# Kernel optimization log

Hardware: AMD Instinct MI355X
Metric: run time of the kernel (lower is better)

The kernel has to match this reference:

```python
import jax, jax.numpy as jnp
import numpy as np

B, D, H = 131072, 8, 128  # batch, input_size (condition dims), hidden_size
DROPOUT_PROB = 0.1
NAN_FRAC = 0.15


def setup_inputs() -> dict:
    key = jax.random.key(0)
    k1, k2, k3, k4, k5, k6 = jax.random.split(key, 6)
    labels = jax.random.normal(k1, (B, D), dtype=jnp.float32)
    # NaN marks 'missing condition' -> falls back to embedding table row
    nan_mask = jax.random.uniform(k2, (B, D)) < NAN_FRAC
    labels = jnp.where(nan_mask, jnp.nan, labels)
    emb_w = jax.random.normal(k3, (D, H), dtype=jnp.float32) * 0.02  # embedding_drop.weight
    w1 = jax.random.normal(k4, (D, H), dtype=jnp.float32)           # Linear(1,H).weight per dim
    b1 = jax.random.normal(k5, (D, H), dtype=jnp.float32) * 0.02    # Linear(1,H).bias per dim
    w2 = jax.random.normal(k6, (D, H, H), dtype=jnp.float32) * 0.08 # Linear(H,H,bias=False).weight [out,in]
    return {"labels": labels, "emb_w": emb_w, "w1": w1, "b1": b1, "w2": w2,
            "train": 0, "unconditioned": 0}


def reference(labels, emb_w, w1, b1, w2, train, unconditioned):
    # drop mask per (sample, dim): NaN labels, optional random dropout, or everything
    if unconditioned:
        drop = jnp.ones(labels.shape, dtype=bool)
    else:
        drop = jnp.isnan(labels)
        if train:
            rkey = jax.random.fold_in(jax.random.key(0), 1)
            drop = drop | (jax.random.uniform(rkey, labels.shape) < DROPOUT_PROB)
    safe = jnp.where(drop, 0.0, labels)                      # [B,D] NaN-free
    # per-dim MLP, vectorized over dims: Linear(1,H) -> softmax(H) -> Linear(H,H)
    h1 = safe[:, :, None] * w1[None, :, :] + b1[None, :, :]  # [B,D,H]
    s = jax.nn.softmax(h1, axis=-1)                          # softmax over hidden (dim=1 of [N,H])
    mlp = jnp.einsum('bdh,dkh->bdk', s, w2)                  # [B,D,H]
    emb = jnp.where(drop[:, :, None], emb_w[None, :, :], mlp)
    if train:
        nkey = jax.random.fold_in(jax.random.key(0), 2)
        emb = emb + jax.random.normal(nkey, emb.shape, dtype=emb.dtype)
    return emb.sum(axis=1)                                   # [B,H]
```

## Files before the change

### kernel.cpp

```cpp
#include <hip/hip_runtime.h>
#include <hip/hip_bf16.h>

typedef __attribute__((ext_vector_type(4))) float f32x4;
typedef __attribute__((ext_vector_type(4))) int   i32x4;
typedef __attribute__((ext_vector_type(8))) short s16x8;

#define NB 131072
#define ND 8
#define NH 128
#define BROWS 128

#if __has_builtin(__builtin_amdgcn_exp2f)
#define EXP2F(x) __builtin_amdgcn_exp2f(x)
#define PRESCALE 1.4426950408889634f
#else
#define EXP2F(x) __expf(x)
#define PRESCALE 1.0f
#endif

#if __has_builtin(__builtin_amdgcn_rcpf)
#define RCPF(x) __builtin_amdgcn_rcpf(x)
#else
#define RCPF(x) (1.0f / (x))
#endif

__device__ __forceinline__ unsigned short f2bf(float f){
  unsigned u = __float_as_uint(f);
  u += 0x7fffu + ((u >> 16) & 1u);
  return (unsigned short)(u >> 16);
}

__device__ __forceinline__ unsigned pk2(float lo, float hi){
  return __builtin_amdgcn_perm(__float_as_uint(hi), __float_as_uint(lo), 0x07060302u);
}

__global__ __launch_bounds__(256) void cvt_w2_kernel(const float* __restrict__ src,
                                                     uint4* __restrict__ dst){
  int i = blockIdx.x * 256 + threadIdx.x;
  int d = i >> 11, kb = (i >> 7) & 15, n = i & 127;
  const float* s = src + ((d * 128 + n) * 128 + kb * 8);
  float4 v0 = ((const float4*)s)[0];
  float4 v1 = ((const float4*)s)[1];
  uint4 o;
  o.x = (unsigned)f2bf(v0.x) | ((unsigned)f2bf(v0.y) << 16);
  o.y = (unsigned)f2bf(v0.z) | ((unsigned)f2bf(v0.w) << 16);
  o.z = (unsigned)f2bf(v1.x) | ((unsigned)f2bf(v1.y) << 16);
  o.w = (unsigned)f2bf(v1.z) | ((unsigned)f2bf(v1.w) << 16);
  dst[i] = o;
}

__global__ __launch_bounds__(256, 3) void cond_embed_kernel(
    const float* __restrict__ labels,
    const float* __restrict__ emb_w,
    const float* __restrict__ w1,
    const float* __restrict__ b1,
    const unsigned short* __restrict__ w2b,
    const int* __restrict__ uncond_p,
    float* __restrict__ out)
{
  __shared__ __align__(16) unsigned short lds_w2[NH * NH];
  __shared__ __align__(16) float lds_lab[ND * BROWS];
  __shared__ __align__(16) float lds_w1[ND * NH];
  __shared__ __align__(16) float lds_b1[ND * NH];
  __shared__ __align__(16) unsigned short lds_embT[NH * 8];

  const int tid  = threadIdx.x;
  const int wave = tid >> 6;
  const int lane = tid & 63;
  const int quad = lane >> 4;
  const int l16  = lane & 15;
  const int uncond = uncond_p[0];
  const int blockbase = blockIdx.x * BROWS;

  {
    float4 v = ((const float4*)(labels + blockbase * ND))[tid];
    int row = tid >> 1, dbase = (tid & 1) * 4;
    lds_lab[(dbase + 0) * BROWS + row] = v.x;
    lds_lab[(dbase + 1) * BROWS + row] = v.y;
    lds_lab[(dbase + 2) * BROWS + row] = v.z;
    lds_lab[(dbase + 3) * BROWS + row] = v.w;
  }
  {
    float4 a = ((const float4*)w1)[tid];
    float4 b = ((const float4*)b1)[tid];
    ((float4*)lds_w1)[tid] = (float4){a.x * PRESCALE, a.y * PRESCALE, a.z * PRESCALE, a.w * PRESCALE};
    ((float4*)lds_b1)[tid] = (float4){b.x * PRESCALE, b.y * PRESCALE, b.z * PRESCALE, b.w * PRESCALE};
  }
  if (tid < NH){
    unsigned e0 = f2bf(emb_w[0*NH + tid]), e1 = f2bf(emb_w[1*NH + tid]);
    unsigned e2 = f2bf(emb_w[2*NH + tid]), e3 = f2bf(emb_w[3*NH + tid]);
    unsigned e4 = f2bf(emb_w[4*NH + tid]), e5 = f2bf(emb_w[5*NH + tid]);
    unsigned e6 = f2bf(emb_w[6*NH + tid]), e7 = f2bf(emb_w[7*NH + tid]);
    uint4 v;
    v.x = e0 | (e1 << 16);  v.y = e2 | (e3 << 16);
    v.z = e4 | (e5 << 16);  v.w = e6 | (e7 << 16);
    ((uint4*)lds_embT)[tid] = v;
  }

  f32x4 acc[2][8];
  #pragma unroll
  for (int mt = 0; mt < 2; ++mt)
    #pragma unroll
    for (int nt = 0; nt < 8; ++nt)
      acc[mt][nt] = (f32x4){0.f, 0.f, 0.f, 0.f};

  const s16x8 bones = (s16x8)((short)0x3F80);

  for (int d = 0; d < ND; ++d){
    __syncthreads();
    {
      const unsigned short* g = w2b + d * (NH * NH);
      #pragma unroll
      for (int i = 0; i < 8; ++i){
        int idx = tid + i * 256;
        __builtin_amdgcn_global_load_lds(
            (const __attribute__((address_space(1))) void*)(g + idx * 8),
            (__attribute__((address_space(3))) void*)(lds_w2 + idx * 8),
            16, 0, 0);
      }
    }
    __syncthreads();

    s16x8 afrag[2][4];
    f32x4 zr[2];
    #pragma unroll
    for (int mt = 0; mt < 2; ++mt){
      int rib = wave * 32 + mt * 16 + l16;
      float x = lds_lab[d * BROWS + rib];
      bool dropA = (uncond != 0) || (x != x);
      float xs = dropA ? 0.f : x;
      #pragma unroll
      for (int t = 0; t < 4; ++t){
        const float* w1p = &lds_w1[d * NH + t * 32 + quad * 8];
        const float* b1p = &lds_b1[d * NH + t * 32 + quad * 8];
        float e0 = EXP2F(fmaf(xs, w1p[0], b1p[0]));
        float e1 = EXP2F(fmaf(xs, w1p[1], b1p[1]));
        float e2 = EXP2F(fmaf(xs, w1p[2], b1p[2]));
        float e3 = EXP2F(fmaf(xs, w1p[3], b1p[3]));
        float e4 = EXP2F(fmaf(xs, w1p[4], b1p[4]));
        float e5 = EXP2F(fmaf(xs, w1p[5], b1p[5]));
        float e6 = EXP2F(fmaf(xs, w1p[6], b1p[6]));
        float e7 = EXP2F(fmaf(xs, w1p[7], b1p[7]));
        i32x4 ai;
        ai[0] = (int)pk2(e0, e1);
        ai[1] = (int)pk2(e2, e3);
        ai[2] = (int)pk2(e4, e5);
        ai[3] = (int)pk2(e6, e7);
        afrag[mt][t] = __builtin_bit_cast(s16x8, ai);
      }
      f32x4 z = (f32x4){0.f, 0.f, 0.f, 0.f};
      #pragma unroll
      for (int t = 0; t < 4; ++t)
        z = __builtin_amdgcn_mfma_f32_16x16x32_bf16(afrag[mt][t], bones, z, 0, 0, 0);
      float4 xc = *(const float4*)&lds_lab[d * BROWS + wave * 32 + mt * 16 + quad * 4];
      f32x4 zi;
      zi[0] = ((uncond != 0) || (xc.x != xc.x)) ? 0.f : RCPF(z[0]);
      zi[1] = ((uncond != 0) || (xc.y != xc.y)) ? 0.f : RCPF(z[1]);
      zi[2] = ((uncond != 0) || (xc.z != xc.z)) ? 0.f : RCPF(z[2]);
      zi[3] = ((uncond != 0) || (xc.w != xc.w)) ? 0.f : RCPF(z[3]);
      zr[mt] = zi;
    }

    #pragma unroll
    for (int nt = 0; nt < 8; ++nt){
      const unsigned short* bb = lds_w2 + (quad * NH + nt * 16 + l16) * 8;
      f32x4 t0 = (f32x4){0.f,0.f,0.f,0.f};
      f32x4 t1 = (f32x4){0.f,0.f,0.f,0.f};
      #pragma unroll
      for (int t = 0; t < 4; ++t){
        s16x8 b = *((const s16x8*)(bb + t * 4 * NH * 8));
        t0 = __builtin_amdgcn_mfma_f32_16x16x32_bf16(afrag[0][t], b, t0, 0, 0, 0);
        t1 = __builtin_amdgcn_mfma_f32_16x16x32_bf16(afrag[1][t], b, t1, 0, 0, 0);
      }
      #pragma unroll
      for (int r = 0; r < 4; ++r){
        acc[0][nt][r] = fmaf(t0[r], zr[0][r], acc[0][nt][r]);
        acc[1][nt][r] = fmaf(t1[r], zr[1][r], acc[1][nt][r]);
      }
    }
  }

  s16x8 aex[2];
  #pragma unroll
  for (int mt = 0; mt < 2; ++mt){
    s16x8 a = (s16x8)((short)0);
    if (quad == 0){
      int rib = wave * 32 + mt * 16 + l16;
      #pragma unroll
      for (int j = 0; j < 8; ++j){
        float x = lds_lab[j * BROWS + rib];
        bool drop = (uncond != 0) || (x != x);
        a[j] = drop ? (short)0x3F80 : (short)0;
      }
    }
    aex[mt] = a;
  }
  #pragma unroll
  for (int nt = 0; nt < 8; ++nt){
    s16x8 b = (s16x8)((short)0);
    if (quad == 0) b = *((const s16x8*)&lds_embT[(nt * 16 + l16) * 8]);
    acc[0][nt] = __builtin_amdgcn_mfma_f32_16x16x32_bf16(aex[0], b, acc[0][nt], 0, 0, 0);
    acc[1][nt] = __builtin_amdgcn_mfma_f32_16x16x32_bf16(aex[1], b, acc[1][nt], 0, 0, 0);
  }

  #pragma unroll
  for (int mt = 0; mt < 2; ++mt){
    #pragma unroll
    for (int nt = 0; nt < 8; ++nt){
      #pragma unroll
      for (int r = 0; r < 4; ++r){
        int row = blockbase + wave * 32 + mt * 16 + quad * 4 + r;
        out[row * NH + nt * 16 + l16] = acc[mt][nt][r];
      }
    }
  }
}

extern "C" void kernel_launch(void* const* d_in, const int* in_sizes, int n_in,
                              void* d_out, int out_size, void* d_ws, size_t ws_size,
                              hipStream_t stream){
  const float* labels = (const float*)d_in[0];
  const float* emb_w  = (const float*)d_in[1];
  const float* w1     = (const float*)d_in[2];
  const float* b1     = (const float*)d_in[3];
  const float* w2     = (const float*)d_in[4];
  const int*   uncond = (const int*)d_in[6];
  (void)in_sizes; (void)n_in; (void)out_size; (void)ws_size;

  float* out = (float*)d_out;
  unsigned short* w2b = (unsigned short*)d_ws;

  cvt_w2_kernel<<<64, 256, 0, stream>>>(w2, (uint4*)w2b);
  cond_embed_kernel<<<NB / BROWS, 256, 0, stream>>>(labels, emb_w, w1, b1, w2b, uncond, out);
}
```

Before: 132.6 us.

## Double-buffer W2 slices and process 256 rows per block

Doubles rows per block (each wave handles 64 rows with four M-tiles) so every W2 B-fragment loaded from LDS feeds four MFMAs instead of two, and halves the number of blocks that each reload all of W2. The W2 slice for the next condition dim is prefetched into a second LDS buffer while the current one is computed, removing one barrier per iteration. Embedding table conversion moves into a separate tiny kernel writing to workspace. This costs more accumulator registers (occupancy hint drops from 3 to 2 blocks per CU) and more LDS.

Measured after the change: 160.7 us. 21.2% more time.

```diff
diff --git a/kernel.cpp b/kernel.cpp
--- a/kernel.cpp
+++ b/kernel.cpp
@@ -8,13 +8,15 @@
 #define NB 131072
 #define ND 8
 #define NH 128
-#define BROWS 128
+#define BROWS 256
+#define MT 4
 
 #if __has_builtin(__builtin_amdgcn_exp2f)
 #define EXP2F(x) __builtin_amdgcn_exp2f(x)
 #define PRESCALE 1.4426950408889634f
 #else
 #define EXP2F(x) __expf(x)
+#define PRESESCALE_FALLBACK
 #define PRESCALE 1.0f
 #endif
 
@@ -49,20 +51,31 @@
   dst[i] = o;
 }
 
-__global__ __launch_bounds__(256, 3) void cond_embed_kernel(
+__global__ void cvt_emb_kernel(const float* __restrict__ emb_w, uint4* __restrict__ dst){
+  int n = threadIdx.x;
+  unsigned e0 = f2bf(emb_w[0*NH + n]), e1 = f2bf(emb_w[1*NH + n]);
+  unsigned e2 = f2bf(emb_w[2*NH + n]), e3 = f2bf(emb_w[3*NH + n]);
+  unsigned e4 = f2bf(emb_w[4*NH + n]), e5 = f2bf(emb_w[5*NH + n]);
+  unsigned e6 = f2bf(emb_w[6*NH + n]), e7 = f2bf(emb_w[7*NH + n]);
+  uint4 v;
+  v.x = e0 | (e1 << 16);  v.y = e2 | (e3 << 16);
+  v.z = e4 | (e5 << 16);  v.w = e6 | (e7 << 16);
+  dst[n] = v;
+}
+
+__global__ __launch_bounds__(256, 2) void cond_embed_kernel(
     const float* __restrict__ labels,
-    const float* __restrict__ emb_w,
     const float* __restrict__ w1,
     const float* __restrict__ b1,
     const unsigned short* __restrict__ w2b,
+    const unsigned short* __restrict__ embT,
     const int* __restrict__ uncond_p,
     float* __restrict__ out)
 {
-  __shared__ __align__(16) unsigned short lds_w2[NH * NH];
+  __shared__ __align__(16) unsigned short lds_w2[2][NH * NH];
   __shared__ __align__(16) float lds_lab[ND * BROWS];
   __shared__ __align__(16) float lds_w1[ND * NH];
   __shared__ __align__(16) float lds_b1[ND * NH];
-  __shared__ __align__(16) unsigned short lds_embT[NH * 8];
 
   const int tid  = threadIdx.x;
   const int wave = tid >> 6;
@@ -73,12 +86,17 @@
   const int blockbase = blockIdx.x * BROWS;
 
   {
-    float4 v = ((const float4*)(labels + blockbase * ND))[tid];
-    int row = tid >> 1, dbase = (tid & 1) * 4;
-    lds_lab[(dbase + 0) * BROWS + row] = v.x;
-    lds_lab[(dbase + 1) * BROWS + row] = v.y;
-    lds_lab[(dbase + 2) * BROWS + row] = v.z;
-    lds_lab[(dbase + 3) * BROWS + row] = v.w;
+    const float4* src = (const float4*)(labels + blockbase * ND);
+    #pragma unroll
+    for (int c = 0; c < 2; ++c){
+      int i = tid + c * 256;
+      float4 v = src[i];
+      int row = i >> 1, db = (i & 1) * 4;
+      lds_lab[(db + 0) * BROWS + row] = v.x;
+      lds_lab[(db + 1) * BROWS + row] = v.y;
+      lds_lab[(db + 2) * BROWS + row] = v.z;
+      lds_lab[(db + 3) * BROWS + row] = v.w;
+    }
   }
   {
     float4 a = ((const float4*)w1)[tid];
@@ -86,20 +104,25 @@
     ((float4*)lds_w1)[tid] = (float4){a.x * PRESCALE, a.y * PRESCALE, a.z * PRESCALE, a.w * PRESCALE};
     ((float4*)lds_b1)[tid] = (float4){b.x * PRESCALE, b.y * PRESCALE, b.z * PRESCALE, b.w * PRESCALE};
   }
-  if (tid < NH){
-    unsigned e0 = f2bf(emb_w[0*NH + tid]), e1 = f2bf(emb_w[1*NH + tid]);
-    unsigned e2 = f2bf(emb_w[2*NH + tid]), e3 = f2bf(emb_w[3*NH + tid]);
-    unsigned e4 = f2bf(emb_w[4*NH + tid]), e5 = f2bf(emb_w[5*NH + tid]);
-    unsigned e6 = f2bf(emb_w[6*NH + tid]), e7 = f2bf(emb_w[7*NH + tid]);
-    uint4 v;
-    v.x = e0 | (e1 << 16);  v.y = e2 | (e3 << 16);
-    v.z = e4 | (e5 << 16);  v.w = e6 | (e7 << 16);
-    ((uint4*)lds_embT)[tid] = v;
-  }
-
-  f32x4 acc[2][8];
-  #pragma unroll
-  for (int mt = 0; mt < 2; ++mt)
+
+  auto stage = [&](int d, int buf){
+    const unsigned short* g = w2b + d * (NH * NH);
+    #pragma unroll
+    for (int i = 0; i < 8; ++i){
+      int idx = tid + i * 256;
+      __builtin_amdgcn_global_load_lds(
+          (const __attribute__((address_space(1))) void*)(g + idx * 8),
+          (__attribute__((address_space(3))) void*)(&lds_w2[buf][idx * 8]),
+          16, 0, 0);
+    }
+  };
+
+  stage(0, 0);
+  __syncthreads();
+
+  f32x4 acc[MT][8];
+  #pragma unroll
+  for (int mt = 0; mt < MT; ++mt)
     #pragma unroll
     for (int nt = 0; nt < 8; ++nt)
       acc[mt][nt] = (f32x4){0.f, 0.f, 0.f, 0.f};
@@ -107,88 +130,89 @@
   const s16x8 bones = (s16x8)((short)0x3F80);
 
   for (int d = 0; d < ND; ++d){
-    __syncthreads();
-    {
-      const unsigned short* g = w2b + d * (NH * NH);
-      #pragma unroll
-      for (int i = 0; i < 8; ++i){
-        int idx = tid + i * 256;
-        __builtin_amdgcn_global_load_lds(
-            (const __attribute__((address_space(1))) void*)(g + idx * 8),
-            (__attribute__((address_space(3))) void*)(lds_w2 + idx * 8),
-            16, 0, 0);
-      }
-    }
-    __syncthreads();
-
-    s16x8 afrag[2][4];
-    f32x4 zr[2];
-    #pragma unroll
-    for (int mt = 0; mt < 2; ++mt){
-      int rib = wave * 32 + mt * 16 + l16;
-      float x = lds_lab[d * BROWS + rib];
-      bool dropA = (uncond != 0) || (x != x);
-      float xs = dropA ? 0.f : x;
-      #pragma unroll
-      for (int t = 0; t < 4; ++t){
-        const float* w1p = &lds_w1[d * NH + t * 32 + quad * 8];
-        const float* b1p = &lds_b1[d * NH + t * 32 + quad * 8];
-        float e0 = EXP2F(fmaf(xs, w1p[0], b1p[0]));
-        float e1 = EXP2F(fmaf(xs, w1p[1], b1p[1]));
-        float e2 = EXP2F(fmaf(xs, w1p[2], b1p[2]));
-        float e3 = EXP2F(fmaf(xs, w1p[3], b1p[3]));
-        float e4 = EXP2F(fmaf(xs, w1p[4], b1p[4]));
-        float e5 = EXP2F(fmaf(xs, w1p[5], b1p[5]));
-        float e6 = EXP2F(fmaf(xs, w1p[6], b1p[6]));
-        float e7 = EXP2F(fmaf(xs, w1p[7], b1p[7]));
+    const int buf = d & 1;
+    if (d < ND - 1) stage(d + 1, buf ^ 1);
+
+    float xs[MT];
+    #pragma unroll
+    for (int mt = 0; mt < MT; ++mt){
+      float x = lds_lab[d * BROWS + wave * 64 + mt * 16 + l16];
+      bool drop = (uncond != 0) || (x != x);
+      xs[mt] = drop ? 0.f : x;
+    }
+
+    s16x8 af[MT][4];
+    #pragma unroll
+    for (int t = 0; t < 4; ++t){
+      const float4* w1q = (const float4*)&lds_w1[d * NH + t * 32 + quad * 8];
+      const float4* b1q = (const float4*)&lds_b1[d * NH + t * 32 + quad * 8];
+      float4 wa = w1q[0], wb = w1q[1];
+      float4 ba = b1q[0], bb = b1q[1];
+      #pragma unroll
+      for (int mt = 0; mt < MT; ++mt){
+        float x = xs[mt];
+        float e0 = EXP2F(fmaf(x, wa.x, ba.x));
+        float e1 = EXP2F(fmaf(x, wa.y, ba.y));
+        float e2 = EXP2F(fmaf(x, wa.z, ba.z));
+        float e3 = EXP2F(fmaf(x, wa.w, ba.w));
+        float e4 = EXP2F(fmaf(x, wb.x, bb.x));
+        float e5 = EXP2F(fmaf(x, wb.y, bb.y));
+        float e6 = EXP2F(fmaf(x, wb.z, bb.z));
+        float e7 = EXP2F(fmaf(x, wb.w, bb.w));
         i32x4 ai;
         ai[0] = (int)pk2(e0, e1);
         ai[1] = (int)pk2(e2, e3);
         ai[2] = (int)pk2(e4, e5);
         ai[3] = (int)pk2(e6, e7);
-        afrag[mt][t] = __builtin_bit_cast(s16x8, ai);
-      }
+        af[mt][t] = __builtin_bit_cast(s16x8, ai);
+      }
+    }
+
+    f32x4 zr[MT];
+    #pragma unroll
+    for (int mt = 0; mt < MT; ++mt){
       f32x4 z = (f32x4){0.f, 0.f, 0.f, 0.f};
       #pragma unroll
       for (int t = 0; t < 4; ++t)
-        z = __builtin_amdgcn_mfma_f32_16x16x32_bf16(afrag[mt][t], bones, z, 0, 0, 0);
-      float4 xc = *(const float4*)&lds_lab[d * BROWS + wave * 32 + mt * 16 + quad * 4];
-      f32x4 zi;
-      zi[0] = ((uncond != 0) || (xc.x != xc.x)) ? 0.f : RCPF(z[0]);
-      zi[1] = ((uncond != 0) || (xc.y != xc.y)) ? 0.f : RCPF(z[1]);
-      zi[2] = ((uncond != 0) || (xc.z != xc.z)) ? 0.f : RCPF(z[2]);
-      zi[3] = ((uncond != 0) || (xc.w != xc.w)) ? 0.f : RCPF(z[3]);
-      zr[mt] = zi;
+        z = __builtin_amdgcn_mfma_f32_16x16x32_bf16(af[mt][t], bones, z, 0, 0, 0);
+      float4 xc = *(const float4*)&lds_lab[d * BROWS + wave * 64 + mt * 16 + quad * 4];
+      zr[mt][0] = ((uncond != 0) || (xc.x != xc.x)) ? 0.f : RCPF(z[0]);
+      zr[mt][1] = ((uncond != 0) || (xc.y != xc.y)) ? 0.f : RCPF(z[1]);
+      zr[mt][2] = ((uncond != 0) || (xc.z != xc.z)) ? 0.f : RCPF(z[2]);
+      zr[mt][3] = ((uncond != 0) || (xc.w != xc.w)) ? 0.f : RCPF(z[3]);
     }
 
     #pragma unroll
     for (int nt = 0; nt < 8; ++nt){
-      const unsigned short* bb = lds_w2 + (quad * NH + nt * 16 + l16) * 8;
-      f32x4 t0 = (f32x4){0.f,0.f,0.f,0.f};
-      f32x4 t1 = (f32x4){0.f,0.f,0.f,0.f};
+      f32x4 tm[MT];
+      #pragma unroll
+      for (int mt = 0; mt < MT; ++mt) tm[mt] = (f32x4){0.f, 0.f, 0.f, 0.f};
       #pragma unroll
       for (int t = 0; t < 4; ++t){
-        s16x8 b = *((const s16x8*)(bb + t * 4 * NH * 8));
-        t0 = __builtin_amdgcn_mfma_f32_16x16x32_bf16(afrag[0][t], b, t0, 0, 0, 0);
-        t1 = __builtin_amdgcn_mfma_f32_16x16x32_bf16(afrag[1][t], b, t1, 0, 0, 0);
-      }
-      #pragma unroll
-      for (int r = 0; r < 4; ++r){
-        acc[0][nt][r] = fmaf(t0[r], zr[0][r], acc[0][nt][r]);
-        acc[1][nt][r] = fmaf(t1[r], zr[1][r], acc[1][nt][r]);
-      }
-    }
-  }
-
-  s16x8 aex[2];
-  #pragma unroll
-  for (int mt = 0; mt < 2; ++mt){
+        s16x8 b = *((const s16x8*)&lds_w2[buf][(t * 512 + quad * 128 + nt * 16 + l16) * 8]);
+        #pragma unroll
+        for (int mt = 0; mt < MT; ++mt)
+          tm[mt] = __builtin_amdgcn_mfma_f32_16x16x32_bf16(af[mt][t], b, tm[mt], 0, 0, 0);
+      }
+      #pragma unroll
+      for (int mt = 0; mt < MT; ++mt)
+        #pragma unroll
+        for (int r = 0; r < 4; ++r)
+          acc[mt][nt][r] = fmaf(tm[mt][r], zr[mt][r], acc[mt][nt][r]);
+    }
+
+    if (d < ND - 1) __syncthreads();
+  }
+
+  s16x8 aex[MT];
+  #pragma unroll
+  for (int mt = 0; mt < MT; ++mt){
     s16x8 a = (s16x8)((short)0);
     if (quad == 0){
-      int rib = wave * 32 + mt * 16 + l16;
+      int row = wave * 64 + mt * 16 + l16;
       #pragma unroll
       for (int j = 0; j < 8; ++j){
-        float x = lds_lab[j * BROWS + rib];
+        float x = lds_lab[j * BROWS + row];
         bool drop = (uncond != 0) || (x != x);
         a[j] = drop ? (short)0x3F80 : (short)0;
       }
@@ -198,18 +222,19 @@
   #pragma unroll
   for (int nt = 0; nt < 8; ++nt){
     s16x8 b = (s16x8)((short)0);
-    if (quad == 0) b = *((const s16x8*)&lds_embT[(nt * 16 + l16) * 8]);
-    acc[0][nt] = __builtin_amdgcn_mfma_f32_16x16x32_bf16(aex[0], b, acc[0][nt], 0, 0, 0);
-    acc[1][nt] = __builtin_amdgcn_mfma_f32_16x16x32_bf16(aex[1], b, acc[1][nt], 0, 0, 0);
-  }
-
-  #pragma unroll
-  for (int mt = 0; mt < 2; ++mt){
+    if (quad == 0) b = __builtin_bit_cast(s16x8, ((const i32x4*)embT)[nt * 16 + l16]);
+    #pragma unroll
+    for (int mt = 0; mt < MT; ++mt)
+      acc[mt][nt] = __builtin_amdgcn_mfma_f32_16x16x32_bf16(aex[mt], b, acc[mt][nt], 0, 0, 0);
+  }
+
+  #pragma unroll
+  for (int mt = 0; mt < MT; ++mt){
     #pragma unroll
     for (int nt = 0; nt < 8; ++nt){
       #pragma unroll
       for (int r = 0; r < 4; ++r){
-        int row = blockbase + wave * 32 + mt * 16 + quad * 4 + r;
+        int row = blockbase + wave * 64 + mt * 16 + quad * 4 + r;
         out[row * NH + nt * 16 + l16] = acc[mt][nt][r];
       }
     }
@@ -228,8 +253,10 @@
   (void)in_sizes; (void)n_in; (void)out_size; (void)ws_size;
 
   float* out = (float*)d_out;
-  unsigned short* w2b = (unsigned short*)d_ws;
+  unsigned short* w2b  = (unsigned short*)d_ws;
+  unsigned short* embT = w2b + ND * NH * NH;
 
   cvt_w2_kernel<<<64, 256, 0, stream>>>(w2, (uint4*)w2b);
-  cond_embed_kernel<<<NB / BROWS, 256, 0, stream>>>(labels, emb_w, w1, b1, w2b, uncond, out);
-}
+  cvt_emb_kernel<<<1, 128, 0, stream>>>(emb_w, (uint4*)embT);
+  cond_embed_kernel<<<NB / BROWS, 256, 0, stream>>>(labels, w1, b1, w2b, embT, uncond, out);
+}
```
